# Performance work log

Hardware: AMD Instinct MI355X
Metric: run time of the kernel (lower is better)

The kernel has to match this reference:

```python
import jax, jax.numpy as jnp
import numpy as np

N = 50000   # nodes
E = 600000  # edges
D = 128     # in_channels
H = 32      # MLP hidden


def setup_inputs() -> dict:
    key = jax.random.key(0)
    ks = jax.random.split(key, 10)
    x = jax.random.normal(ks[0], (N, D), dtype=jnp.float32)
    edge_index = jax.random.randint(ks[1], (2, E), 0, N, dtype=jnp.int32)
    W_gcn = jax.random.normal(ks[2], (D, D), dtype=jnp.float32) / np.sqrt(D)
    b_gcn = jnp.zeros((D,), dtype=jnp.float32)
    w1 = jax.random.normal(ks[3], (D, H), dtype=jnp.float32) / np.sqrt(D)
    b1 = jnp.zeros((H,), dtype=jnp.float32)
    w2 = jax.random.normal(ks[4], (H, H), dtype=jnp.float32) / np.sqrt(H)
    b2 = jnp.zeros((H,), dtype=jnp.float32)
    w3 = jax.random.normal(ks[5], (H, 1), dtype=jnp.float32) / np.sqrt(H)
    b3 = jnp.zeros((1,), dtype=jnp.float32)
    return {"x": x, "edge_index": edge_index, "W_gcn": W_gcn, "b_gcn": b_gcn,
            "w1": w1, "b1": b1, "w2": w2, "b2": b2, "w3": w3, "b3": b3}


def _gcn_conv(x, edge_index, W, b):
    """PyG GCNConv: add self-loops, symmetric D^-1/2 (A+I) D^-1/2 normalization."""
    xw = x @ W  # [N, D]
    loop = jnp.arange(N, dtype=edge_index.dtype)
    row = jnp.concatenate([edge_index[0], loop])  # source
    col = jnp.concatenate([edge_index[1], loop])  # target
    deg = jax.ops.segment_sum(jnp.ones_like(col, dtype=xw.dtype), col, num_segments=N)
    dinv = jnp.where(deg > 0, jax.lax.rsqrt(deg), 0.0)
    norm = dinv[row] * dinv[col]              # [E+N]
    msg = xw[row] * norm[:, None]             # gather + scale, [E+N, D]
    out = jax.ops.segment_sum(msg, col, num_segments=N)  # scatter-add, [N, D]
    return out + b


def reference(x, edge_index, W_gcn, b_gcn, w1, b1, w2, b2, w3, b3):
    out = jax.nn.relu(_gcn_conv(x, edge_index, W_gcn, b_gcn))
    h = out + x                               # residual
    h = jax.nn.relu(h @ w1 + b1)
    h = jax.nn.relu(h @ w2 + b2)
    return h @ w3 + b3                        # [N, 1]
```

## Files before the change

kernel.cpp:

```cpp
#include <hip/hip_runtime.h>

#define DIM 128
#define HID 32
#define CAP 64

typedef __attribute__((ext_vector_type(8))) short v8s;
typedef __attribute__((ext_vector_type(4))) float v4f;

static __device__ __forceinline__ unsigned short f2bf(float f) {
    unsigned int u = __float_as_uint(f);
    u += 0x7fffu + ((u >> 16) & 1u);
    return (unsigned short)(u >> 16);
}

__global__ __launch_bounds__(256) void prep_kernel(int* __restrict__ cnt,
                                                   const float* __restrict__ W,
                                                   unsigned short* __restrict__ wbt,
                                                   int n, int nz) {
    int t = threadIdx.x;
    if ((int)blockIdx.x < nz) {
        int i0 = (blockIdx.x << 10) + t * 4;
        if (i0 + 3 < n) {
            *(int4*)&cnt[i0] = make_int4(0, 0, 0, 0);
        } else {
            for (int i = i0; i < n; ++i) cnt[i] = 0;
        }
    } else {
        int base = (blockIdx.x - nz) * 2048 + t * 8;
#pragma unroll
        for (int i = 0; i < 8; ++i) {
            int f = base + i;
            int k = f >> 7, nn = f & 127;
            wbt[nn * 128 + k] = f2bf(W[f]);
        }
    }
}

__global__ __launch_bounds__(256) void gemm_fill_kernel(const float* __restrict__ x,
                                                        const unsigned short* __restrict__ wbt,
                                                        signed char* __restrict__ xwq,
                                                        float* __restrict__ sc,
                                                        const int* __restrict__ ei,
                                                        int* __restrict__ cnt,
                                                        unsigned short* __restrict__ srcs,
                                                        int n, int E, int ngemm) {
    int t = threadIdx.x;
    if ((int)blockIdx.x < ngemm) {
        int row0 = blockIdx.x * 64;
        int w = t >> 6;
        int l = t & 63;
        int q = l >> 4;
        int mn = l & 15;
        int row = row0 + w * 16 + mn;
        v8s afrag[4];
        if (row < n) {
            const float* xr = x + (size_t)row * DIM;
#pragma unroll
            for (int kt = 0; kt < 4; ++kt) {
                const float4* xp = (const float4*)(xr + kt * 32 + q * 8);
                float4 qa = xp[0], qb = xp[1];
                v8s pk;
                pk[0] = (short)f2bf(qa.x); pk[1] = (short)f2bf(qa.y);
                pk[2] = (short)f2bf(qa.z); pk[3] = (short)f2bf(qa.w);
                pk[4] = (short)f2bf(qb.x); pk[5] = (short)f2bf(qb.y);
                pk[6] = (short)f2bf(qb.z); pk[7] = (short)f2bf(qb.w);
                afrag[kt] = pk;
            }
        } else {
#pragma unroll
            for (int kt = 0; kt < 4; ++kt) afrag[kt] = (v8s){0,0,0,0,0,0,0,0};
        }
        v4f acc[8];
#pragma unroll
        for (int ct = 0; ct < 8; ++ct) {
            acc[ct] = (v4f){0.f, 0.f, 0.f, 0.f};
#pragma unroll
            for (int kt = 0; kt < 4; ++kt) {
                v8s bfrag = *(const v8s*)&wbt[(ct * 16 + mn) * 128 + kt * 32 + q * 8];
                acc[ct] = __builtin_amdgcn_mfma_f32_16x16x32_bf16(afrag[kt], bfrag, acc[ct], 0, 0, 0);
            }
        }
        float m[4];
#pragma unroll
        for (int i = 0; i < 4; ++i) {
            float mm = 0.f;
#pragma unroll
            for (int ct = 0; ct < 8; ++ct) mm = fmaxf(mm, fabsf(acc[ct][i]));
            m[i] = mm;
        }
#pragma unroll
        for (int off = 1; off < 16; off <<= 1) {
#pragma unroll
            for (int i = 0; i < 4; ++i) m[i] = fmaxf(m[i], __shfl_xor(m[i], off));
        }
        float inv[4];
#pragma unroll
        for (int i = 0; i < 4; ++i) {
            m[i] = fmaxf(m[i], 1e-20f);
            inv[i] = 127.0f / m[i];
        }
        if (mn == 0) {
#pragma unroll
            for (int i = 0; i < 4; ++i) {
                int rowg = row0 + w * 16 + q * 4 + i;
                if (rowg < n) sc[rowg] = m[i] * (1.0f / 127.0f);
            }
        }
#pragma unroll
        for (int ct = 0; ct < 8; ++ct) {
            int colg = ct * 16 + mn;
#pragma unroll
            for (int i = 0; i < 4; ++i) {
                int rowg = row0 + w * 16 + q * 4 + i;
                if (rowg < n)
                    xwq[(size_t)rowg * DIM + colg] =
                        (signed char)__float2int_rn(acc[ct][i] * inv[i]);
            }
        }
    } else {
        const int* col = ei + E;
        int base = ((blockIdx.x - ngemm) * 256 + t) * 4;
        if (base + 3 < E) {
            int4 r4 = *(const int4*)&ei[base];
            int4 c4 = *(const int4*)&col[base];
            int p0 = atomicAdd(&cnt[c4.x], 1);
            int p1 = atomicAdd(&cnt[c4.y], 1);
            int p2 = atomicAdd(&cnt[c4.z], 1);
            int p3 = atomicAdd(&cnt[c4.w], 1);
            if (p0 < CAP) __builtin_nontemporal_store((unsigned short)r4.x, &srcs[(c4.x << 6) + p0]);
            if (p1 < CAP) __builtin_nontemporal_store((unsigned short)r4.y, &srcs[(c4.y << 6) + p1]);
            if (p2 < CAP) __builtin_nontemporal_store((unsigned short)r4.z, &srcs[(c4.z << 6) + p2]);
            if (p3 < CAP) __builtin_nontemporal_store((unsigned short)r4.w, &srcs[(c4.w << 6) + p3]);
        } else {
            for (int e = base; e < E; ++e) {
                int r = ei[e], c = col[e];
                int p = atomicAdd(&cnt[c], 1);
                if (p < CAP) __builtin_nontemporal_store((unsigned short)r, &srcs[(c << 6) + p]);
            }
        }
    }
}

__global__ __launch_bounds__(256) void dw_kernel(const int* __restrict__ cnt,
                                                 const float* __restrict__ sc,
                                                 float* __restrict__ dw, int n) {
    int i0 = (blockIdx.x * 256 + threadIdx.x) * 4;
    if (i0 + 3 < n) {
        int4 c4 = *(const int4*)&cnt[i0];
        float4 s4 = *(const float4*)&sc[i0];
        float4 w4;
        w4.x = rsqrtf((float)c4.x + 1.0f) * s4.x;
        w4.y = rsqrtf((float)c4.y + 1.0f) * s4.y;
        w4.z = rsqrtf((float)c4.z + 1.0f) * s4.z;
        w4.w = rsqrtf((float)c4.w + 1.0f) * s4.w;
        *(float4*)&dw[i0] = w4;
    } else {
        for (int i = i0; i < n; ++i) dw[i] = rsqrtf((float)cnt[i] + 1.0f) * sc[i];
    }
}

__global__ __launch_bounds__(256) void gather_tail_kernel(
    const signed char* __restrict__ xwq, const float* __restrict__ x,
    const int* __restrict__ cnt, const unsigned short* __restrict__ srcs,
    const float* __restrict__ dw, const float* __restrict__ sc,
    const float* __restrict__ b_gcn,
    const float* __restrict__ w1, const float* __restrict__ b1,
    const float* __restrict__ w2, const float* __restrict__ b2,
    const float* __restrict__ w3, const float* __restrict__ b3,
    float* __restrict__ out, int n) {
    __shared__ float hs[8][132];
    __shared__ float t1s[8][40];
    int t = threadIdx.x;
    int g = t >> 5, j = t & 31;
    int node = blockIdx.x * 8 + g;

    if (node < n) {
        int dtrue = cnt[node];
        int d = min(dtrue, CAP);
        int beg = node << 6;
        int aq = ((const int*)(xwq + (size_t)node * DIM))[j];
        float scn = sc[node];
        float4 xv = ((const float4*)(x + (size_t)node * DIM))[j];
        float4 bg = ((const float4*)b_gcn)[j];
        float ax = 0.f, ay = 0.f, az = 0.f, aw = 0.f;
        for (int c0 = 0; c0 < d; c0 += 32) {
            int sj = 0; float wj = 0.f;
            if (c0 + j < d) {
                sj = (int)srcs[beg + c0 + j];
                wj = dw[sj];
            }
            int m = min(32, d - c0);
            int i = 0;
            for (; i + 8 <= m; i += 8) {
                int v[8]; float wgt[8];
#pragma unroll
                for (int u = 0; u < 8; ++u) {
                    int src = __shfl(sj, i + u, 32);
                    wgt[u] = __shfl(wj, i + u, 32);
                    v[u] = ((const int*)(xwq + (size_t)src * DIM))[j];
                }
#pragma unroll
                for (int u = 0; u < 8; ++u) {
                    ax += wgt[u] * (float)((v[u] << 24) >> 24);
                    ay += wgt[u] * (float)((v[u] << 16) >> 24);
                    az += wgt[u] * (float)((v[u] <<  8) >> 24);
                    aw += wgt[u] * (float)( v[u]        >> 24);
                }
            }
            for (; i + 4 <= m; i += 4) {
                int v[4]; float wgt[4];
#pragma unroll
                for (int u = 0; u < 4; ++u) {
                    int src = __shfl(sj, i + u, 32);
                    wgt[u] = __shfl(wj, i + u, 32);
                    v[u] = ((const int*)(xwq + (size_t)src * DIM))[j];
                }
#pragma unroll
                for (int u = 0; u < 4; ++u) {
                    ax += wgt[u] * (float)((v[u] << 24) >> 24);
                    ay += wgt[u] * (float)((v[u] << 16) >> 24);
                    az += wgt[u] * (float)((v[u] <<  8) >> 24);
                    aw += wgt[u] * (float)( v[u]        >> 24);
                }
            }
            for (; i < m; ++i) {
                int src = __shfl(sj, i, 32);
                float w = __shfl(wj, i, 32);
                int v0 = ((const int*)(xwq + (size_t)src * DIM))[j];
                ax += w * (float)((v0 << 24) >> 24);
                ay += w * (float)((v0 << 16) >> 24);
                az += w * (float)((v0 <<  8) >> 24);
                aw += w * (float)( v0        >> 24);
            }
        }
        float di = rsqrtf((float)dtrue + 1.0f);
        float sself = di * di * scn;
        float* h = &hs[g][4 * j];
        h[0] = fmaxf(di * ax + sself * (float)((aq << 24) >> 24) + bg.x, 0.f) + xv.x;
        h[1] = fmaxf(di * ay + sself * (float)((aq << 16) >> 24) + bg.y, 0.f) + xv.y;
        h[2] = fmaxf(di * az + sself * (float)((aq <<  8) >> 24) + bg.z, 0.f) + xv.z;
        h[3] = fmaxf(di * aw + sself * (float)( aq        >> 24) + bg.w, 0.f) + xv.w;
        float acc = b1[j];
        for (int k = 0; k < DIM; k += 4) {
            float4 hv = *(const float4*)&hs[g][k];
            acc += hv.x * w1[(k + 0) * HID + j];
            acc += hv.y * w1[(k + 1) * HID + j];
            acc += hv.z * w1[(k + 2) * HID + j];
            acc += hv.w * w1[(k + 3) * HID + j];
        }
        t1s[g][j] = fmaxf(acc, 0.0f);
        acc = b2[j];
        for (int k = 0; k < HID; k += 4) {
            float4 tv = *(const float4*)&t1s[g][k];
            acc += tv.x * w2[(k + 0) * HID + j];
            acc += tv.y * w2[(k + 1) * HID + j];
            acc += tv.z * w2[(k + 2) * HID + j];
            acc += tv.w * w2[(k + 3) * HID + j];
        }
        float v = fmaxf(acc, 0.0f) * w3[j];
#pragma unroll
        for (int off = 16; off > 0; off >>= 1) v += __shfl_down(v, off, 32);
        if (j == 0) out[node] = v + b3[0];
    }
}

extern "C" void kernel_launch(void* const* d_in, const int* in_sizes, int n_in,
                              void* d_out, int out_size, void* d_ws, size_t ws_size,
                              hipStream_t stream) {
    const float* x     = (const float*)d_in[0];
    const int*   ei    = (const int*)d_in[1];
    const float* W_gcn = (const float*)d_in[2];
    const float* b_gcn = (const float*)d_in[3];
    const float* w1    = (const float*)d_in[4];
    const float* b1    = (const float*)d_in[5];
    const float* w2    = (const float*)d_in[6];
    const float* b2    = (const float*)d_in[7];
    const float* w3    = (const float*)d_in[8];
    const float* b3    = (const float*)d_in[9];
    float* out = (float*)d_out;

    const int n = in_sizes[0] / DIM;
    const int E = in_sizes[1] / 2;

    char* ws = (char*)d_ws;
    signed char* xwq = (signed char*)ws;
    char* p = ws + (size_t)n * DIM;
    p = (char*)(((size_t)p + 15) & ~(size_t)15);
    float* sc   = (float*)p;         p += (size_t)n * sizeof(float);
    float* dw   = (float*)p;         p += (size_t)n * sizeof(float);
    int*   cnt  = (int*)p;           p += (size_t)n * sizeof(int);
    p = (char*)(((size_t)p + 255) & ~(size_t)255);
    unsigned short* srcs = (unsigned short*)p;
    p += (size_t)n * CAP * sizeof(unsigned short);
    unsigned short* wbt = (unsigned short*)p;

    const int nz     = (n + 1023) / 1024;
    const int ngemm  = (n + 63) / 64;
    const int nfill  = (E + 1023) / 1024;

    prep_kernel<<<nz + 8, 256, 0, stream>>>(cnt, W_gcn, wbt, n, nz);
    gemm_fill_kernel<<<ngemm + nfill, 256, 0, stream>>>(x, wbt, xwq, sc, ei,
                                                        cnt, srcs, n, E, ngemm);
    dw_kernel<<<(n + 1023) / 1024, 256, 0, stream>>>(cnt, sc, dw, n);
    gather_tail_kernel<<<(n + 7) / 8, 256, 0, stream>>>(xwq, x, cnt, srcs, dw, sc,
                                                        b_gcn, w1, b1, w2, b2,
                                                        w3, b3, out, n);
}
```

Before: 173.3 us.

## Fold residual x@w1 into the GCN GEMM and drop x reload in tail

Uses linearity (relu(gcn)+x)@w1 = relu(gcn)@w1 + x@w1 to compute x@w1 as two extra MFMA column tiles in the existing bf16 GEMM. The result goes to a new fp32 [N,32] buffer that the tail kernel adds to its first-layer accumulator, so the tail no longer rereads the full fp32 x rows (512 B per node) and reads 128 B per node instead. The weight prep kernel now writes a combined transposed bf16 [160,128] weight. It also switches the edge-slot stores from nontemporal to ordinary stores. The cost is x@w1 computed in bf16 rather than fp32, plus extra register pressure from 10 accumulator tiles.

```diff
diff --git a/kernel.cpp b/kernel.cpp
--- a/kernel.cpp
+++ b/kernel.cpp
@@ -15,6 +15,7 @@
 
 __global__ __launch_bounds__(256) void prep_kernel(int* __restrict__ cnt,
                                                    const float* __restrict__ W,
+                                                   const float* __restrict__ w1,
                                                    unsigned short* __restrict__ wbt,
                                                    int n, int nz) {
     int t = threadIdx.x;
@@ -30,8 +31,9 @@
 #pragma unroll
         for (int i = 0; i < 8; ++i) {
             int f = base + i;
-            int k = f >> 7, nn = f & 127;
-            wbt[nn * 128 + k] = f2bf(W[f]);
+            int nn = f >> 7, k = f & 127;
+            float v = (nn < 128) ? W[k * 128 + nn] : w1[k * HID + (nn - 128)];
+            wbt[f] = f2bf(v);
         }
     }
 }
@@ -40,6 +42,7 @@
                                                         const unsigned short* __restrict__ wbt,
                                                         signed char* __restrict__ xwq,
                                                         float* __restrict__ sc,
+                                                        float* __restrict__ xw1,
                                                         const int* __restrict__ ei,
                                                         int* __restrict__ cnt,
                                                         unsigned short* __restrict__ srcs,
@@ -70,9 +73,9 @@
 #pragma unroll
             for (int kt = 0; kt < 4; ++kt) afrag[kt] = (v8s){0,0,0,0,0,0,0,0};
         }
-        v4f acc[8];
-#pragma unroll
-        for (int ct = 0; ct < 8; ++ct) {
+        v4f acc[10];
+#pragma unroll
+        for (int ct = 0; ct < 10; ++ct) {
             acc[ct] = (v4f){0.f, 0.f, 0.f, 0.f};
 #pragma unroll
             for (int kt = 0; kt < 4; ++kt) {
@@ -115,6 +118,15 @@
                 if (rowg < n)
                     xwq[(size_t)rowg * DIM + colg] =
                         (signed char)__float2int_rn(acc[ct][i] * inv[i]);
+            }
+        }
+#pragma unroll
+        for (int ct = 8; ct < 10; ++ct) {
+            int colg = (ct - 8) * 16 + mn;
+#pragma unroll
+            for (int i = 0; i < 4; ++i) {
+                int rowg = row0 + w * 16 + q * 4 + i;
+                if (rowg < n) xw1[(size_t)rowg * HID + colg] = acc[ct][i];
             }
         }
     } else {
@@ -127,15 +139,15 @@
             int p1 = atomicAdd(&cnt[c4.y], 1);
             int p2 = atomicAdd(&cnt[c4.z], 1);
             int p3 = atomicAdd(&cnt[c4.w], 1);
-            if (p0 < CAP) __builtin_nontemporal_store((unsigned short)r4.x, &srcs[(c4.x << 6) + p0]);
-            if (p1 < CAP) __builtin_nontemporal_store((unsigned short)r4.y, &srcs[(c4.y << 6) + p1]);
-            if (p2 < CAP) __builtin_nontemporal_store((unsigned short)r4.z, &srcs[(c4.z << 6) + p2]);
-            if (p3 < CAP) __builtin_nontemporal_store((unsigned short)r4.w, &srcs[(c4.w << 6) + p3]);
+            if (p0 < CAP) srcs[(c4.x << 6) + p0] = (unsigned short)r4.x;
+            if (p1 < CAP) srcs[(c4.y << 6) + p1] = (unsigned short)r4.y;
+            if (p2 < CAP) srcs[(c4.z << 6) + p2] = (unsigned short)r4.z;
+            if (p3 < CAP) srcs[(c4.w << 6) + p3] = (unsigned short)r4.w;
         } else {
             for (int e = base; e < E; ++e) {
                 int r = ei[e], c = col[e];
                 int p = atomicAdd(&cnt[c], 1);
-                if (p < CAP) __builtin_nontemporal_store((unsigned short)r, &srcs[(c << 6) + p]);
+                if (p < CAP) srcs[(c << 6) + p] = (unsigned short)r;
             }
         }
     }
@@ -160,10 +172,10 @@
 }
 
 __global__ __launch_bounds__(256) void gather_tail_kernel(
-    const signed char* __restrict__ xwq, const float* __restrict__ x,
+    const signed char* __restrict__ xwq,
     const int* __restrict__ cnt, const unsigned short* __restrict__ srcs,
     const float* __restrict__ dw, const float* __restrict__ sc,
-    const float* __restrict__ b_gcn,
+    const float* __restrict__ xw1, const float* __restrict__ b_gcn,
     const float* __restrict__ w1, const float* __restrict__ b1,
     const float* __restrict__ w2, const float* __restrict__ b2,
     const float* __restrict__ w3, const float* __restrict__ b3,
@@ -180,7 +192,6 @@
         int beg = node << 6;
         int aq = ((const int*)(xwq + (size_t)node * DIM))[j];
         float scn = sc[node];
-        float4 xv = ((const float4*)(x + (size_t)node * DIM))[j];
         float4 bg = ((const float4*)b_gcn)[j];
         float ax = 0.f, ay = 0.f, az = 0.f, aw = 0.f;
         for (int c0 = 0; c0 < d; c0 += 32) {
@@ -236,11 +247,11 @@
         float di = rsqrtf((float)dtrue + 1.0f);
         float sself = di * di * scn;
         float* h = &hs[g][4 * j];
-        h[0] = fmaxf(di * ax + sself * (float)((aq << 24) >> 24) + bg.x, 0.f) + xv.x;
-        h[1] = fmaxf(di * ay + sself * (float)((aq << 16) >> 24) + bg.y, 0.f) + xv.y;
-        h[2] = fmaxf(di * az + sself * (float)((aq <<  8) >> 24) + bg.z, 0.f) + xv.z;
-        h[3] = fmaxf(di * aw + sself * (float)( aq        >> 24) + bg.w, 0.f) + xv.w;
-        float acc = b1[j];
+        h[0] = fmaxf(di * ax + sself * (float)((aq << 24) >> 24) + bg.x, 0.f);
+        h[1] = fmaxf(di * ay + sself * (float)((aq << 16) >> 24) + bg.y, 0.f);
+        h[2] = fmaxf(di * az + sself * (float)((aq <<  8) >> 24) + bg.z, 0.f);
+        h[3] = fmaxf(di * aw + sself * (float)( aq        >> 24) + bg.w, 0.f);
+        float acc = b1[j] + xw1[(size_t)node * HID + j];
         for (int k = 0; k < DIM; k += 4) {
             float4 hv = *(const float4*)&hs[g][k];
             acc += hv.x * w1[(k + 0) * HID + j];
@@ -292,17 +303,18 @@
     p = (char*)(((size_t)p + 255) & ~(size_t)255);
     unsigned short* srcs = (unsigned short*)p;
     p += (size_t)n * CAP * sizeof(unsigned short);
+    float* xw1g = (float*)p;         p += (size_t)n * HID * sizeof(float);
     unsigned short* wbt = (unsigned short*)p;
 
     const int nz     = (n + 1023) / 1024;
     const int ngemm  = (n + 63) / 64;
     const int nfill  = (E + 1023) / 1024;
 
-    prep_kernel<<<nz + 8, 256, 0, stream>>>(cnt, W_gcn, wbt, n, nz);
-    gemm_fill_kernel<<<ngemm + nfill, 256, 0, stream>>>(x, wbt, xwq, sc, ei,
+    prep_kernel<<<nz + 10, 256, 0, stream>>>(cnt, W_gcn, w1, wbt, n, nz);
+    gemm_fill_kernel<<<ngemm + nfill, 256, 0, stream>>>(x, wbt, xwq, sc, xw1g, ei,
                                                         cnt, srcs, n, E, ngemm);
     dw_kernel<<<(n + 1023) / 1024, 256, 0, stream>>>(cnt, sc, dw, n);
-    gather_tail_kernel<<<(n + 7) / 8, 256, 0, stream>>>(xwq, x, cnt, srcs, dw, sc,
-                                                        b_gcn, w1, b1, w2, b2,
+    gather_tail_kernel<<<(n + 7) / 8, 256, 0, stream>>>(xwq, cnt, srcs, dw, sc,
+                                                        xw1g, b_gcn, w1, b1, w2, b2,
                                                         w3, b3, out, n);
 }
```

Measured after the change: 192.7 us. 11.2% more time.
